# Kernel tuning notes

Hardware: AMD Instinct MI355X
Metric: run time of the kernel (lower is better)

## Reference

```python
import jax, jax.numpy as jnp
import numpy as np

NUM_HEADS = 32
HEAD_DIM = 128
ROPE_DIM = 64
HIDDEN = 4096
C_KV = 512
C_Q = 1536
CACHE_LEN = 4096
BATCH = 4


def _apply_rope(x, positions):
    # x: [B, S, H, R]; interleaved rotate-half RoPE at given absolute positions
    R = x.shape[-1]
    inv_freq = 1.0 / (10000.0 ** (jnp.arange(0, R, 2, dtype=jnp.float32) / R))
    ang = positions[:, None].astype(jnp.float32) * inv_freq[None, :]  # [S, R/2]
    cos = jnp.cos(ang)[None, :, None, :]
    sin = jnp.sin(ang)[None, :, None, :]
    x1, x2 = x[..., 0::2], x[..., 1::2]
    out = jnp.stack([x1 * cos - x2 * sin, x1 * sin + x2 * cos], axis=-1)
    return out.reshape(x.shape).astype(x.dtype)


def setup_inputs() -> dict:
    key = jax.random.key(0)
    ks = jax.random.split(key, 12)
    s = lambda fan: 1.0 / np.sqrt(fan)
    return {
        "hidden_states": jax.random.normal(ks[0], (BATCH, 1, HIDDEN), jnp.float32),
        "mask": jnp.zeros((BATCH, 1, 1, CACHE_LEN + 1), jnp.float32),
        "cached_c_KV": jax.random.normal(ks[1], (BATCH, CACHE_LEN, C_KV), jnp.float32),
        "cached_k_R": jax.random.normal(ks[2], (BATCH, CACHE_LEN, ROPE_DIM), jnp.float32),
        "W_DKV": jax.random.normal(ks[3], (HIDDEN, C_KV), jnp.float32) * s(HIDDEN),
        "W_UK": jax.random.normal(ks[4], (C_KV, NUM_HEADS * HEAD_DIM), jnp.float32) * s(C_KV),
        "W_UV": jax.random.normal(ks[5], (C_KV, NUM_HEADS * HEAD_DIM), jnp.float32) * s(C_KV),
        "W_DQ": jax.random.normal(ks[6], (HIDDEN, C_Q), jnp.float32) * s(HIDDEN),
        "W_UQ": jax.random.normal(ks[7], (C_Q, NUM_HEADS * HEAD_DIM), jnp.float32) * s(C_Q),
        "W_QR": jax.random.normal(ks[8], (C_Q, NUM_HEADS * ROPE_DIM), jnp.float32) * s(C_Q),
        "W_KR": jax.random.normal(ks[9], (HIDDEN, ROPE_DIM), jnp.float32) * s(HIDDEN),
        "W_O": jax.random.normal(ks[10], (NUM_HEADS * HEAD_DIM, HIDDEN), jnp.float32) * s(NUM_HEADS * HEAD_DIM),
    }


def reference(hidden_states, mask, cached_c_KV, cached_k_R,
              W_DKV, W_UK, W_UV, W_DQ, W_UQ, W_QR, W_KR, W_O):
    B = hidden_states.shape[0]
    S_cache = cached_c_KV.shape[1]
    scale = 1.0 / np.sqrt(HEAD_DIM + ROPE_DIM)

    # latent projections for current token
    c_KV = hidden_states @ W_DKV                      # [B,1,C_KV]
    k_C = (c_KV @ W_UK).reshape(B, 1, NUM_HEADS, HEAD_DIM)
    v_C = (c_KV @ W_UV).reshape(B, 1, NUM_HEADS, HEAD_DIM)
    c_Q = hidden_states @ W_DQ                        # [B,1,C_Q]
    q_C = (c_Q @ W_UQ).reshape(B, 1, NUM_HEADS, HEAD_DIM)
    q_R = (c_Q @ W_QR).reshape(B, 1, NUM_HEADS, ROPE_DIM)
    k_R = (hidden_states @ W_KR).reshape(B, 1, 1, ROPE_DIM)

    # RoPE at the current decode position (= cache length)
    pos = jnp.array([S_cache], dtype=jnp.int32)
    q_R = _apply_rope(q_R, pos)
    k_R_cur = _apply_rope(k_R, pos)
    k_R_cur = jnp.broadcast_to(k_R_cur, (B, 1, NUM_HEADS, ROPE_DIM))

    q = jnp.concatenate([q_C, q_R], axis=-1)          # [B,1,H,D+R]
    k_cur = jnp.concatenate([k_C, k_R_cur], axis=-1)  # [B,1,H,D+R]

    # re-up-project cached latents (the expensive MLA decode step)
    cached_k_C = (cached_c_KV @ W_UK).reshape(B, S_cache, NUM_HEADS, HEAD_DIM)
    cached_v_C = (cached_c_KV @ W_UV).reshape(B, S_cache, NUM_HEADS, HEAD_DIM)
    cached_k_R_exp = jnp.broadcast_to(cached_k_R[:, :, None, :],
                                      (B, S_cache, NUM_HEADS, ROPE_DIM))
    cached_k = jnp.concatenate([cached_k_C, cached_k_R_exp], axis=-1)

    k = jnp.concatenate([cached_k, k_cur], axis=1)    # [B,S+1,H,D+R]
    v = jnp.concatenate([cached_v_C, v_C], axis=1)    # [B,S+1,H,D]

    # single-query attention: scores [B,H,1,S+1]
    scores = jnp.einsum('bqhd,bkhd->bhqk', q, k) * scale
    scores = scores + mask * -1e9
    probs = jax.nn.softmax(scores, axis=-1)
    attn = jnp.einsum('bhqk,bkhd->bqhd', probs, v).reshape(B, 1, NUM_HEADS * HEAD_DIM)

    out = attn @ W_O                                  # [B,1,HIDDEN]
    new_cached_c_KV = jnp.concatenate([cached_c_KV, c_KV], axis=1)
    new_cached_k_R = jnp.concatenate([cached_k_R, k_R_cur[:, :, 0, :]], axis=1)
    return out, new_cached_c_KV, new_cached_k_R
```

## Files before the change

### kernel.cpp

```cpp
#include <hip/hip_runtime.h>
#include <math.h>

#define NB 4
#define HID 4096
#define CKV 512
#define CQ 1536
#define NH 32
#define HD 128
#define RD 64
#define SS 4096
#define SK 4097
#define SKP 4100

#define SCALE_F 0.07216878364870322f

#define NP1 64
#define NP2 24
#define NPV 32
#define NUV 16
#define NWO 32

#define KD   576
#define QKB_STR 584

typedef __attribute__((ext_vector_type(8))) short short8v;
typedef __attribute__((ext_vector_type(4))) float f32x4;

enum : int {
  WS_QABS  = 0,
  WS_QROPE = WS_QABS + NB*NH*CKV,
  WS_KROPE = WS_QROPE + NB*NH*RD,
  WS_CKV   = WS_KROPE + NB*RD,
  WS_CQ    = WS_CKV + NB*CKV,
  WS_SCA   = WS_CQ + NB*CQ,
  WS_P1    = WS_SCA + NB*NH*SKP,
  WS_P2    = WS_P1 + NP1*NB*528*4,
  WS_OPART = WS_P2 + NP2*NB*6144,
  WS_UVPART= WS_OPART + NPV*NB*NH*CKV,
  WS_WOPART= WS_UVPART + NUV*NB*HID,
  WS_KVBF  = WS_WOPART + NWO*NB*HID,
  WS_QBF   = WS_KVBF + (NB*SK*KD)/2,
  WS_TOTAL = WS_QBF + (NB*NH*KD)/2
};

__device__ inline void fma4(float4& a, float s, const float4& v) {
  a.x += s*v.x; a.y += s*v.y; a.z += s*v.z; a.w += s*v.w;
}
__device__ inline float dot4(const float4& a, const float4& b) {
  return a.x*b.x + a.y*b.y + a.z*b.z + a.w*b.w;
}
__device__ inline unsigned short f2bf(float f) {
  union { float f; unsigned int u; } v; v.f = f;
  unsigned int r = v.u + 0x7FFFu + ((v.u >> 16) & 1u);
  return (unsigned short)(r >> 16);
}
__device__ inline ushort4 f2bf4(float4 v) {
  ushort4 r; r.x = f2bf(v.x); r.y = f2bf(v.y); r.z = f2bf(v.z); r.w = f2bf(v.w);
  return r;
}

__global__ __launch_bounds__(256)
void k_proj1copy(const float* __restrict__ hidden,
                 const float* __restrict__ Wdkv,
                 const float* __restrict__ Wdq,
                 const float* __restrict__ Wkr,
                 float* __restrict__ ws,
                 const float4* __restrict__ src_ckv,
                 const float4* __restrict__ src_kr,
                 float4* __restrict__ dst_ckv,
                 float4* __restrict__ dst_kr) {
  __shared__ float4 red_s[4][NB][64];
  unsigned short* kvbf = (unsigned short*)(ws + WS_KVBF);
  const int bx = blockIdx.x;
  if (bx < 576) {
    const int gx = bx % 9, gy = bx / 9;
    const int lane = threadIdx.x & 63, ksub = threadIdx.x >> 6;
    const int col4 = gx * 64 + lane;
    const int k0 = gy * 64 + ksub * 16;
    const bool valid = col4 < 528;
    float4 acc[NB] = {};
    if (valid) {
      const float* W; int C4, wcol4;
      if (col4 < 128)      { W = Wdkv; C4 = 128; wcol4 = col4; }
      else if (col4 < 512) { W = Wdq;  C4 = 384; wcol4 = col4 - 128; }
      else                 { W = Wkr;  C4 = 16;  wcol4 = col4 - 512; }
      const float4* wp = (const float4*)W + (size_t)k0 * C4 + wcol4;
      #pragma unroll
      for (int i = 0; i < 16; ++i) {
        float4 w4 = wp[(size_t)i * C4];
        #pragma unroll
        for (int b = 0; b < NB; ++b) fma4(acc[b], hidden[b*HID + k0 + i], w4);
      }
    }
    #pragma unroll
    for (int b = 0; b < NB; ++b) red_s[ksub][b][lane] = acc[b];
    __syncthreads();
    if (ksub == 0 && valid) {
      #pragma unroll
      for (int b = 0; b < NB; ++b) {
        float4 s = red_s[0][b][lane];
        #pragma unroll
        for (int j = 1; j < 4; ++j) {
          float4 v = red_s[j][b][lane];
          s.x += v.x; s.y += v.y; s.z += v.z; s.w += v.w;
        }
        *(float4*)(ws + WS_P1 + ((size_t)(gy*NB + b)*528 + col4)*4) = s;
      }
    }
  } else {
    const int bxc = bx - 576;
    if (bxc < 8192) {
      int b = bxc >> 11;
      int idx = (bxc & 2047) * 256 + threadIdx.x;
      float4 v = src_ckv[(size_t)b*(SS*CKV/4) + idx];
      dst_ckv[(size_t)b*(SK*CKV/4) + idx] = v;
      int off = idx * 4;
      int k = off >> 9, c = off & 511;
      *(ushort4*)(kvbf + ((size_t)b*SK + k)*KD + c) = f2bf4(v);
    } else {
      int bx2 = bxc - 8192;
      int b = bx2 >> 8;
      int idx = (bx2 & 255) * 256 + threadIdx.x;
      float4 v = src_kr[(size_t)b*(SS*RD/4) + idx];
      dst_kr[(size_t)b*(SK*RD/4) + idx] = v;
      int off = idx * 4;
      int k = off >> 6, rr = off & 63;
      *(ushort4*)(kvbf + ((size_t)b*SK + k)*KD + 512 + rr) = f2bf4(v);
    }
  }
}

__global__ __launch_bounds__(256)
void k_proj2r1(const float* __restrict__ Wuq,
               const float* __restrict__ Wqr,
               float* __restrict__ ws,
               float* __restrict__ out_ckv,
               float* __restrict__ out_kr) {
  __shared__ float4 red_s[4][NB][64];
  __shared__ float act_s[NB][64];
  unsigned short* kvbf = (unsigned short*)(ws + WS_KVBF);
  const int bx = blockIdx.x;
  const int tid = threadIdx.x;
  if (bx < 576) {
    const int gx = bx % 24, gy = bx / 24;
    {
      const int b = tid >> 6, i = tid & 63;
      const int k = gy * 64 + i;
      const float* base = ws + WS_P1 + (size_t)b*2112 + 512 + k;
      float s = 0.f;
      #pragma unroll 8
      for (int p = 0; p < NP1; ++p) s += base[(size_t)p*NB*2112];
      act_s[b][i] = s;
    }
    __syncthreads();
    const int lane = tid & 63, ksub = tid >> 6;
    const int col4 = gx * 64 + lane;
    const float* W; int C4, wcol4;
    if (col4 < 1024) { W = Wuq; C4 = 1024; wcol4 = col4; }
    else             { W = Wqr; C4 = 512;  wcol4 = col4 - 1024; }
    const float4* wp = (const float4*)W + (size_t)(gy*64 + ksub*16) * C4 + wcol4;
    float4 acc[NB] = {};
    #pragma unroll
    for (int i = 0; i < 16; ++i) {
      float4 w4 = wp[(size_t)i * C4];
      #pragma unroll
      for (int b = 0; b < NB; ++b) fma4(acc[b], act_s[b][ksub*16 + i], w4);
    }
    #pragma unroll
    for (int b = 0; b < NB; ++b) red_s[ksub][b][lane] = acc[b];
    __syncthreads();
    if (ksub == 0) {
      #pragma unroll
      for (int b = 0; b < NB; ++b) {
        float4 s = red_s[0][b][lane];
        #pragma unroll
        for (int j = 1; j < 4; ++j) {
          float4 v = red_s[j][b][lane];
          s.x += v.x; s.y += v.y; s.z += v.z; s.w += v.w;
        }
        *(float4*)(ws + WS_P2 + (size_t)(gy*NB + b)*6144 + col4*4) = s;
      }
    }
  } else {
    const int w = (bx - 576) * 256 + tid;
    if (w >= 528*NB) return;
    const int b = w / 528, col4 = w % 528;
    float4 s = {};
    #pragma unroll 8
    for (int p = 0; p < NP1; ++p) {
      float4 v = *(const float4*)(ws + WS_P1 + ((size_t)(p*NB + b)*528 + col4)*4);
      s.x += v.x; s.y += v.y; s.z += v.z; s.w += v.w;
    }
    if (col4 < 128) {
      *(float4*)(ws + WS_CKV + b*CKV + col4*4) = s;
      *(float4*)(out_ckv + (size_t)b*SK*CKV + (size_t)SS*CKV + col4*4) = s;
      *(ushort4*)(kvbf + ((size_t)b*SK + SS)*KD + col4*4) = f2bf4(s);
    } else if (col4 < 512) {
      *(float4*)(ws + WS_CQ + b*CQ + (col4 - 128)*4) = s;
    } else {
      const int c0 = (col4 - 512) * 4;
      const double LN1E4 = 9.210340371976184;
      int i0 = c0 >> 1;
      double a0 = 4096.0 * exp(-(double)i0 / 32.0 * LN1E4);
      double a1 = 4096.0 * exp(-(double)(i0 + 1) / 32.0 * LN1E4);
      float c0f = (float)cos(a0), s0f = (float)sin(a0);
      float c1f = (float)cos(a1), s1f = (float)sin(a1);
      float4 o;
      o.x = s.x*c0f - s.y*s0f;  o.y = s.x*s0f + s.y*c0f;
      o.z = s.z*c1f - s.w*s1f;  o.w = s.z*s1f + s.w*c1f;
      *(float4*)(ws + WS_KROPE + b*RD + c0) = o;
      *(float4*)(out_kr + (size_t)b*SK*RD + (size_t)SS*RD + c0) = o;
      *(ushort4*)(kvbf + ((size_t)b*SK + SS)*KD + 512 + c0) = f2bf4(o);
    }
  }
}

__global__ __launch_bounds__(256)
void k_absorb_rope(const float* __restrict__ Wuk,
                   float* __restrict__ ws) {
  unsigned short* qbf = (unsigned short*)(ws + WS_QBF);
  const int bid = blockIdx.x, tid = threadIdx.x;
  if (bid < 256) {
    const int h = bid >> 3, cq = bid & 7;
    __shared__ float qc_s[NB][HD];
    __shared__ float part_s[NB][256];
    for (int e = tid; e < NB*HD; e += 256) {
      int b = e >> 7, d = e & 127;
      float v = 0.f;
      #pragma unroll
      for (int p = 0; p < NP2; ++p)
        v += ws[WS_P2 + (size_t)(p*NB + b)*6144 + h*HD + d];
      qc_s[b][d] = v;
    }
    __syncthreads();
    const int c = cq*64 + (tid & 63);
    const int dg = tid >> 6;
    const float4* wrow = (const float4*)(Wuk + (size_t)c*(NH*HD) + h*HD + dg*32);
    float acc[NB] = {0,0,0,0};
    #pragma unroll
    for (int d4 = 0; d4 < 8; ++d4) {
      float4 w4 = wrow[d4];
      #pragma unroll
      for (int b = 0; b < NB; ++b)
        acc[b] += dot4(w4, *(const float4*)&qc_s[b][dg*32 + d4*4]);
    }
    #pragma unroll
    for (int b = 0; b < NB; ++b) part_s[b][tid] = acc[b];
    __syncthreads();
    if (tid < 64) {
      #pragma unroll
      for (int b = 0; b < NB; ++b) {
        float v = (part_s[b][tid] + part_s[b][tid+64] + part_s[b][tid+128] + part_s[b][tid+192]) * SCALE_F;
        ws[WS_QABS + (size_t)(b*NH + h)*CKV + cq*64 + tid] = v;
        qbf[(size_t)(b*NH + h)*KD + cq*64 + tid] = f2bf(v);
      }
    }
  } else {
    const int b = bid - 256;
    const double LN1E4 = 9.210340371976184;
    for (int pid = tid; pid < NH*32; pid += 256) {
      int h = pid >> 5, i = pid & 31;
      float x1 = 0.f, x2 = 0.f;
      #pragma unroll
      for (int p = 0; p < NP2; ++p) {
        const float* base = ws + WS_P2 + (size_t)(p*NB + b)*6144 + 4096 + h*RD + 2*i;
        x1 += base[0]; x2 += base[1];
      }
      double ang = 4096.0 * exp(-(double)i / 32.0 * LN1E4);
      float cs = (float)cos(ang), sn = (float)sin(ang);
      float o0 = (x1*cs - x2*sn) * SCALE_F;
      float o1 = (x1*sn + x2*cs) * SCALE_F;
      ws[WS_QROPE + (b*NH + h)*RD + 2*i]     = o0;
      ws[WS_QROPE + (b*NH + h)*RD + 2*i + 1] = o1;
      qbf[(size_t)(b*NH + h)*KD + 512 + 2*i]     = f2bf(o0);
      qbf[(size_t)(b*NH + h)*KD + 512 + 2*i + 1] = f2bf(o1);
    }
  }
}

__global__ __launch_bounds__(256)
void k_scores_mfma(float* __restrict__ ws) {
  __shared__ unsigned short q_s[32 * QKB_STR];
  __shared__ unsigned short kv_s[32 * QKB_STR];
  const unsigned short* kvbf = (const unsigned short*)(ws + WS_KVBF);
  const unsigned short* qbf  = (const unsigned short*)(ws + WS_QBF);
  const int tid = threadIdx.x;
  const int b  = blockIdx.y;
  const int k0 = blockIdx.x * 32;
  {
    const int r = tid >> 3, u0 = tid & 7;
    const unsigned short* qsrc = qbf + (size_t)(b*NH + r)*KD;
    const int k = k0 + r;
    const unsigned short* ksrc = (k <= SS) ? (kvbf + ((size_t)b*SK + k)*KD) : nullptr;
    #pragma unroll
    for (int j = 0; j < 9; ++j) {
      int u = (u0 + 8*j) * 8;
      *(uint4*)&q_s[r*QKB_STR + u] = *(const uint4*)(qsrc + u);
      uint4 kvv = {0u, 0u, 0u, 0u};
      if (ksrc) kvv = *(const uint4*)(ksrc + u);
      *(uint4*)&kv_s[r*QKB_STR + u] = kvv;
    }
  }
  __syncthreads();
  const int wid = tid >> 6, lane = tid & 63;
  const int m0 = (wid & 1) * 16;
  const int n0 = (wid >> 1) * 16;
  const int l15 = lane & 15, lq = lane >> 4;
  const unsigned short* arow = &q_s[(m0 + l15)*QKB_STR + lq*8];
  const unsigned short* brow = &kv_s[(n0 + l15)*QKB_STR + lq*8];
  f32x4 acc = {0.f, 0.f, 0.f, 0.f};
  #pragma unroll
  for (int ks = 0; ks < 18; ++ks) {
    short8v a = *(const short8v*)(arow + ks*32);
    short8v bb = *(const short8v*)(brow + ks*32);
    acc = __builtin_amdgcn_mfma_f32_16x16x32_bf16(a, bb, acc, 0, 0, 0);
  }
  const int key = k0 + n0 + l15;
  if (key <= SS) {
    #pragma unroll
    for (int r = 0; r < 4; ++r) {
      int h = m0 + lq*4 + r;
      ws[WS_SCA + (size_t)(b*NH + h)*SKP + key] = acc[r];
    }
  }
}

__global__ __launch_bounds__(256)
void k_softmax(const float* __restrict__ mask, float* __restrict__ ws) {
  __shared__ float red[256];
  const int tid = threadIdx.x;
  const int b = blockIdx.x >> 5;
  float* sa = ws + WS_SCA + (size_t)blockIdx.x * SKP;
  const float* mrow = mask + (size_t)b * SK;
  float v[17];
  float m = -INFINITY;
  #pragma unroll
  for (int r = 0; r < 17; ++r) {
    int k = tid + r*256;
    v[r] = (k < SK) ? (sa[k] + mrow[k] * (-1e9f)) : -INFINITY;
    m = fmaxf(m, v[r]);
  }
  red[tid] = m; __syncthreads();
  for (int st = 128; st > 0; st >>= 1) {
    if (tid < st) red[tid] = fmaxf(red[tid], red[tid+st]);
    __syncthreads();
  }
  m = red[0]; __syncthreads();
  float e[17];
  float l = 0.f;
  #pragma unroll
  for (int r = 0; r < 17; ++r) {
    int k = tid + r*256;
    e[r] = (k < SK) ? __expf(v[r] - m) : 0.f;
    l += e[r];
  }
  red[tid] = l; __syncthreads();
  for (int st = 128; st > 0; st >>= 1) {
    if (tid < st) red[tid] += red[tid+st];
    __syncthreads();
  }
  float inv = 1.f / red[0];
  #pragma unroll
  for (int r = 0; r < 17; ++r) {
    int k = tid + r*256;
    if (k < SK) sa[k] = e[r] * inv;
  }
}

__global__ __launch_bounds__(256)
void k_pv(const float* __restrict__ kv_cache, float* __restrict__ ws) {
  __shared__ float p_s[32][132];
  const int tid = threadIdx.x;
  const int c4 = tid & 15, hg = tid >> 4;
  const int b  = blockIdx.z;
  const int c  = blockIdx.y * 64 + c4 * 4;
  const int k0 = blockIdx.x * 128;
  #pragma unroll
  for (int j = 0; j < 4; ++j) {
    int e = tid + j*256;
    int h = e >> 5, k4 = e & 31;
    *(float4*)&p_s[h][k4*4] =
        *(const float4*)(ws + WS_SCA + (size_t)(b*NH + h)*SKP + k0 + k4*4);
  }
  __syncthreads();
  const float* kvp = kv_cache + ((size_t)b*SS + k0)*CKV + c;
  float4 acc0 = {}, acc1 = {};
  #pragma unroll 4
  for (int kk = 0; kk < 128; kk += 4) {
    float4 kv4[4];
    #pragma unroll
    for (int j = 0; j < 4; ++j)
      kv4[j] = *(const float4*)(kvp + (size_t)(kk + j)*CKV);
    float4 p4a = *(const float4*)&p_s[hg][kk];
    float4 p4b = *(const float4*)&p_s[hg + 16][kk];
    fma4(acc0, p4a.x, kv4[0]); fma4(acc1, p4b.x, kv4[0]);
    fma4(acc0, p4a.y, kv4[1]); fma4(acc1, p4b.y, kv4[1]);
    fma4(acc0, p4a.z, kv4[2]); fma4(acc1, p4b.z, kv4[2]);
    fma4(acc0, p4a.w, kv4[3]); fma4(acc1, p4b.w, kv4[3]);
  }
  if (blockIdx.x == NPV - 1) {
    float4 kv = *(const float4*)(ws + WS_CKV + b*CKV + c);
    float pa = ws[WS_SCA + (size_t)(b*NH + hg)*SKP + SS];
    float pb = ws[WS_SCA + (size_t)(b*NH + hg + 16)*SKP + SS];
    fma4(acc0, pa, kv);
    fma4(acc1, pb, kv);
  }
  *(float4*)(ws + WS_OPART + (((size_t)blockIdx.x*NB + b)*NH + hg)*CKV + c) = acc0;
  *(float4*)(ws + WS_OPART + (((size_t)blockIdx.x*NB + b)*NH + hg + 16)*CKV + c) = acc1;
}

__global__ __launch_bounds__(256)
void k_uv2(const float* __restrict__ Wuv, float* __restrict__ ws) {
  __shared__ float4 red_s[4][NB][64];
  __shared__ float ol_s[NB][2][32];
  const int tid = threadIdx.x;
  const int x = blockIdx.x & 15, y = blockIdx.x >> 4;
  {
    const int b = tid >> 6, hh = (tid >> 5) & 1, ci = tid & 31;
    const float* base = ws + WS_OPART + ((size_t)b*NH + (2*x + hh))*CKV + y*32 + ci;
    float s = 0.f;
    #pragma unroll 8
    for (int p = 0; p < NPV; ++p) s += base[(size_t)p*(NB*NH*CKV)];
    ol_s[b][hh][ci] = s;
  }
  __syncthreads();
  const int lane = tid & 63, csub = tid >> 6;
  const int col4 = x * 64 + lane;
  const int hh = (col4 >> 5) & 1;
  const float4* wp = (const float4*)Wuv + (size_t)(y*32 + csub*8) * 1024 + col4;
  float4 acc[NB] = {};
  #pragma unroll
  for (int i = 0; i < 8; ++i) {
    float4 w4 = wp[(size_t)i * 1024];
    #pragma unroll
    for (int b = 0; b < NB; ++b)
      fma4(acc[b], ol_s[b][hh][csub*8 + i], w4);
  }
  #pragma unroll
  for (int b = 0; b < NB; ++b) red_s[csub][b][lane] = acc[b];
  __syncthreads();
  if (csub == 0) {
    #pragma unroll
    for (int b = 0; b < NB; ++b) {
      float4 s = red_s[0][b][lane];
      #pragma unroll
      for (int j = 1; j < 4; ++j) {
        float4 v = red_s[j][b][lane];
        s.x += v.x; s.y += v.y; s.z += v.z; s.w += v.w;
      }
      *(float4*)(ws + WS_UVPART + (size_t)(y*NB + b)*HID + col4*4) = s;
    }
  }
}

__global__ __launch_bounds__(256)
void k_wo2(const float* __restrict__ Wo, float* __restrict__ ws) {
  __shared__ float4 red_s[4][NB][64];
  __shared__ float at_s[NB][128];
  const int tid = threadIdx.x;
  const int x = blockIdx.x & 15, y = blockIdx.x >> 4;
  {
    const int b = tid >> 6, q = tid & 63;
    #pragma unroll
    for (int e = 0; e < 2; ++e) {
      int idx = q*2 + e;
      const float* base = ws + WS_UVPART + (size_t)b*HID + y*128 + idx;
      float s = 0.f;
      #pragma unroll
      for (int p = 0; p < NUV; ++p) s += base[(size_t)p*(NB*HID)];
      at_s[b][idx] = s;
    }
  }
  __syncthreads();
  const int lane = tid & 63, ksub = tid >> 6;
  const int col4 = x * 64 + lane;
  const float4* wp = (const float4*)Wo + (size_t)(y*128 + ksub*32) * 1024 + col4;
  float4 acc[NB] = {};
  #pragma unroll 8
  for (int i = 0; i < 32; ++i) {
    float4 w4 = wp[(size_t)i * 1024];
    #pragma unroll
    for (int b = 0; b < NB; ++b)
      fma4(acc[b], at_s[b][ksub*32 + i], w4);
  }
  #pragma unroll
  for (int b = 0; b < NB; ++b) red_s[ksub][b][lane] = acc[b];
  __syncthreads();
  if (ksub == 0) {
    #pragma unroll
    for (int b = 0; b < NB; ++b) {
      float4 s = red_s[0][b][lane];
      #pragma unroll
      for (int j = 1; j < 4; ++j) {
        float4 v = red_s[j][b][lane];
        s.x += v.x; s.y += v.y; s.z += v.z; s.w += v.w;
      }
      *(float4*)(ws + WS_WOPART + (size_t)(y*NB + b)*HID + col4*4) = s;
    }
  }
}

__global__ __launch_bounds__(256)
void k_reduce5(const float* __restrict__ ws, float* __restrict__ out) {
  const int idx = blockIdx.x * 256 + threadIdx.x;
  float4 s = {};
  #pragma unroll 8
  for (int p = 0; p < NWO; ++p) {
    float4 v = *(const float4*)(ws + WS_WOPART + (size_t)p*(NB*HID) + (size_t)idx*4);
    s.x += v.x; s.y += v.y; s.z += v.z; s.w += v.w;
  }
  *(float4*)(out + (size_t)idx*4) = s;
}

extern "C" void kernel_launch(void* const* d_in, const int* in_sizes, int n_in,
                              void* d_out, int out_size, void* d_ws, size_t ws_size,
                              hipStream_t stream) {
  (void)in_sizes; (void)n_in; (void)out_size; (void)ws_size;
  const float* hidden = (const float*)d_in[0];
  const float* mask   = (const float*)d_in[1];
  const float* ckv_c  = (const float*)d_in[2];
  const float* kr_c   = (const float*)d_in[3];
  const float* Wdkv   = (const float*)d_in[4];
  const float* Wuk    = (const float*)d_in[5];
  const float* Wuv    = (const float*)d_in[6];
  const float* Wdq    = (const float*)d_in[7];
  const float* Wuq    = (const float*)d_in[8];
  const float* Wqr    = (const float*)d_in[9];
  const float* Wkr    = (const float*)d_in[10];
  const float* Wo     = (const float*)d_in[11];
  float* out = (float*)d_out;
  float* ws  = (float*)d_ws;
  float* out_ckv = out + NB*HID;
  float* out_kr  = out + NB*HID + (size_t)NB*SK*CKV;

  k_proj1copy<<<9792, 256, 0, stream>>>(hidden, Wdkv, Wdq, Wkr, ws,
                                        (const float4*)ckv_c, (const float4*)kr_c,
                                        (float4*)out_ckv, (float4*)out_kr);
  k_proj2r1<<<585, 256, 0, stream>>>(Wuq, Wqr, ws, out_ckv, out_kr);
  k_absorb_rope<<<260, 256, 0, stream>>>(Wuk, ws);
  k_scores_mfma<<<dim3(129, 4), 256, 0, stream>>>(ws);
  k_softmax<<<NB*NH, 256, 0, stream>>>(mask, ws);
  k_pv<<<dim3(NPV, 8, 4), 256, 0, stream>>>(ckv_c, ws);
  k_uv2<<<256, 256, 0, stream>>>(Wuv, ws);
  k_wo2<<<512, 256, 0, stream>>>(Wo, ws);
  k_reduce5<<<16, 256, 0, stream>>>(ws, out);
}
```

Measured before the change: 112.6 us.

## Fuse scores, softmax and PV into split-K flash-decoding attention kernel

Replaces the separate scores, softmax and fp32 PV kernels with one kernel. Each block computes QK scores for a 128-key chunk with bf16 MFMA, does a local softmax, and multiplies P by the bf16 latent cache with MFMA, storing per-chunk max and sum. The UV kernel then rescales and combines the partial outputs. This removes the global score round-trip, two launches and the fp32 cache read in PV. In exchange, scores are recomputed once per column block (4x), and the probabilities and cache values are rounded to bf16.

```diff
diff --git a/kernel.cpp b/kernel.cpp
--- a/kernel.cpp
+++ b/kernel.cpp
@@ -22,6 +22,10 @@
 
 #define KD   576
 #define QKB_STR 584
+#define PBF_STR 4104
+#define TV_STR 40
+#define SFS  168
+#define PSTR 168
 
 typedef __attribute__((ext_vector_type(8))) short short8v;
 typedef __attribute__((ext_vector_type(4))) float f32x4;
@@ -40,7 +44,8 @@
   WS_WOPART= WS_UVPART + NUV*NB*HID,
   WS_KVBF  = WS_WOPART + NWO*NB*HID,
   WS_QBF   = WS_KVBF + (NB*SK*KD)/2,
-  WS_TOTAL = WS_QBF + (NB*NH*KD)/2
+  WS_ML    = WS_QBF + (NB*NH*KD)/2,
+  WS_TOTAL = WS_ML + NB*NH*NPV*2
 };
 
 __device__ inline void fma4(float4& a, float s, const float4& v) {
@@ -57,6 +62,10 @@
 __device__ inline ushort4 f2bf4(float4 v) {
   ushort4 r; r.x = f2bf(v.x); r.y = f2bf(v.y); r.z = f2bf(v.z); r.w = f2bf(v.w);
   return r;
+}
+__device__ inline float bf2f(unsigned short u) {
+  union { unsigned int u; float f; } v; v.u = ((unsigned int)u) << 16;
+  return v.f;
 }
 
 __global__ __launch_bounds__(256)
@@ -279,134 +288,138 @@
 }
 
 __global__ __launch_bounds__(256)
-void k_scores_mfma(float* __restrict__ ws) {
-  __shared__ unsigned short q_s[32 * QKB_STR];
+void k_attn(const float* __restrict__ mask, float* __restrict__ ws) {
   __shared__ unsigned short kv_s[32 * QKB_STR];
+  __shared__ float S_s[32 * SFS];
+  unsigned short* P_s  = kv_s;
+  unsigned short* kvT_s = kv_s + 32*PSTR;
   const unsigned short* kvbf = (const unsigned short*)(ws + WS_KVBF);
   const unsigned short* qbf  = (const unsigned short*)(ws + WS_QBF);
   const int tid = threadIdx.x;
-  const int b  = blockIdx.y;
-  const int k0 = blockIdx.x * 32;
-  {
-    const int r = tid >> 3, u0 = tid & 7;
-    const unsigned short* qsrc = qbf + (size_t)(b*NH + r)*KD;
-    const int k = k0 + r;
-    const unsigned short* ksrc = (k <= SS) ? (kvbf + ((size_t)b*SK + k)*KD) : nullptr;
-    #pragma unroll
-    for (int j = 0; j < 9; ++j) {
-      int u = (u0 + 8*j) * 8;
-      *(uint4*)&q_s[r*QKB_STR + u] = *(const uint4*)(qsrc + u);
-      uint4 kvv = {0u, 0u, 0u, 0u};
-      if (ksrc) kvv = *(const uint4*)(ksrc + u);
-      *(uint4*)&kv_s[r*QKB_STR + u] = kvv;
-    }
-  }
-  __syncthreads();
+  const int j  = blockIdx.x;
+  const int qy = blockIdx.y;
+  const int b  = blockIdx.z;
+  const int k0 = j * 128;
+  const int NSUB = (j == NPV-1) ? 5 : 4;
   const int wid = tid >> 6, lane = tid & 63;
+  const int l15 = lane & 15, lq = lane >> 4;
+
   const int m0 = (wid & 1) * 16;
   const int n0 = (wid >> 1) * 16;
-  const int l15 = lane & 15, lq = lane >> 4;
-  const unsigned short* arow = &q_s[(m0 + l15)*QKB_STR + lq*8];
-  const unsigned short* brow = &kv_s[(n0 + l15)*QKB_STR + lq*8];
-  f32x4 acc = {0.f, 0.f, 0.f, 0.f};
+  const unsigned short* arow = qbf + (size_t)(b*NH + m0 + l15)*KD + lq*8;
+  for (int sc = 0; sc < NSUB; ++sc) {
+    {
+      const int r = tid >> 3, u0 = tid & 7;
+      const int k = k0 + sc*32 + r;
+      const unsigned short* ksrc = (k <= SS) ? (kvbf + ((size_t)b*SK + k)*KD) : nullptr;
+      #pragma unroll
+      for (int u8 = 0; u8 < 9; ++u8) {
+        int u = (u0 + 8*u8) * 8;
+        uint4 kvv = {0u, 0u, 0u, 0u};
+        if (ksrc) kvv = *(const uint4*)(ksrc + u);
+        *(uint4*)&kv_s[r*QKB_STR + u] = kvv;
+      }
+    }
+    __syncthreads();
+    const unsigned short* brow = &kv_s[(n0 + l15)*QKB_STR + lq*8];
+    f32x4 acc = {0.f, 0.f, 0.f, 0.f};
+    #pragma unroll
+    for (int ks = 0; ks < 18; ++ks) {
+      short8v a = *(const short8v*)(arow + ks*32);
+      short8v bb = *(const short8v*)(brow + ks*32);
+      acc = __builtin_amdgcn_mfma_f32_16x16x32_bf16(a, bb, acc, 0, 0, 0);
+    }
+    const int kk = sc*32 + n0 + l15;
+    const bool vkey = (k0 + kk) <= SS;
+    #pragma unroll
+    for (int r = 0; r < 4; ++r)
+      S_s[(m0 + lq*4 + r)*SFS + kk] = vkey ? acc[r] : -1e30f;
+    __syncthreads();
+  }
+
+  {
+    const int row = tid >> 3, i8 = tid & 7;
+    const int NK = NSUB * 32;
+    float m = -INFINITY;
+    for (int kk = i8; kk < NK; kk += 8) {
+      int kgl = k0 + kk;
+      float mv = (kgl < SK) ? mask[(size_t)b*SK + kgl] : 0.f;
+      float v = S_s[row*SFS + kk] + mv * (-1e9f);
+      S_s[row*SFS + kk] = v;
+      m = fmaxf(m, v);
+    }
+    m = fmaxf(m, __shfl_xor(m, 1));
+    m = fmaxf(m, __shfl_xor(m, 2));
+    m = fmaxf(m, __shfl_xor(m, 4));
+    float l = 0.f;
+    for (int kk = i8; kk < NK; kk += 8) {
+      float e = __expf(S_s[row*SFS + kk] - m);
+      l += e;
+      P_s[row*PSTR + kk] = f2bf(e);
+    }
+    l += __shfl_xor(l, 1);
+    l += __shfl_xor(l, 2);
+    l += __shfl_xor(l, 4);
+    if (i8 == 0 && qy == 0) {
+      float* ml = ws + WS_ML + ((size_t)(b*NH + row)*NPV + j)*2;
+      ml[0] = m; ml[1] = l;
+    }
+  }
+  __syncthreads();
+
+  const int c0 = qy * 128;
+  f32x4 acc4[4] = {{0,0,0,0},{0,0,0,0},{0,0,0,0},{0,0,0,0}};
+  const int kk_st = tid & 31, cgrp = tid >> 5;
+  for (int sc = 0; sc < NSUB; ++sc) {
+    {
+      const int k = k0 + sc*32 + kk_st;
+      ushort4 v0 = {0,0,0,0}, v1 = {0,0,0,0}, v2 = {0,0,0,0}, v3 = {0,0,0,0};
+      if (k <= SS) {
+        const unsigned short* src = kvbf + ((size_t)b*SK + k)*KD + c0 + cgrp*16;
+        v0 = *(const ushort4*)(src);
+        v1 = *(const ushort4*)(src + 4);
+        v2 = *(const ushort4*)(src + 8);
+        v3 = *(const ushort4*)(src + 12);
+      }
+      int cb = cgrp*16;
+      kvT_s[(cb+ 0)*TV_STR + kk_st] = v0.x;
+      kvT_s[(cb+ 1)*TV_STR + kk_st] = v0.y;
+      kvT_s[(cb+ 2)*TV_STR + kk_st] = v0.z;
+      kvT_s[(cb+ 3)*TV_STR + kk_st] = v0.w;
+      kvT_s[(cb+ 4)*TV_STR + kk_st] = v1.x;
+      kvT_s[(cb+ 5)*TV_STR + kk_st] = v1.y;
+      kvT_s[(cb+ 6)*TV_STR + kk_st] = v1.z;
+      kvT_s[(cb+ 7)*TV_STR + kk_st] = v1.w;
+      kvT_s[(cb+ 8)*TV_STR + kk_st] = v2.x;
+      kvT_s[(cb+ 9)*TV_STR + kk_st] = v2.y;
+      kvT_s[(cb+10)*TV_STR + kk_st] = v2.z;
+      kvT_s[(cb+11)*TV_STR + kk_st] = v2.w;
+      kvT_s[(cb+12)*TV_STR + kk_st] = v3.x;
+      kvT_s[(cb+13)*TV_STR + kk_st] = v3.y;
+      kvT_s[(cb+14)*TV_STR + kk_st] = v3.z;
+      kvT_s[(cb+15)*TV_STR + kk_st] = v3.w;
+    }
+    __syncthreads();
+    short8v a = *(const short8v*)(&P_s[(m0 + l15)*PSTR + sc*32 + lq*8]);
+    #pragma unroll
+    for (int t = 0; t < 4; ++t) {
+      const int nt = (wid >> 1) + 2*t;
+      const unsigned short* brow = &kvT_s[(nt*16 + l15)*TV_STR + lq*8];
+      short8v bb = *(const short8v*)(brow);
+      acc4[t] = __builtin_amdgcn_mfma_f32_16x16x32_bf16(a, bb, acc4[t], 0, 0, 0);
+    }
+    __syncthreads();
+  }
   #pragma unroll
-  for (int ks = 0; ks < 18; ++ks) {
-    short8v a = *(const short8v*)(arow + ks*32);
-    short8v bb = *(const short8v*)(brow + ks*32);
-    acc = __builtin_amdgcn_mfma_f32_16x16x32_bf16(a, bb, acc, 0, 0, 0);
-  }
-  const int key = k0 + n0 + l15;
-  if (key <= SS) {
+  for (int t = 0; t < 4; ++t) {
+    const int nt = (wid >> 1) + 2*t;
+    const int c = c0 + nt*16 + l15;
     #pragma unroll
     for (int r = 0; r < 4; ++r) {
       int h = m0 + lq*4 + r;
-      ws[WS_SCA + (size_t)(b*NH + h)*SKP + key] = acc[r];
-    }
-  }
-}
-
-__global__ __launch_bounds__(256)
-void k_softmax(const float* __restrict__ mask, float* __restrict__ ws) {
-  __shared__ float red[256];
-  const int tid = threadIdx.x;
-  const int b = blockIdx.x >> 5;
-  float* sa = ws + WS_SCA + (size_t)blockIdx.x * SKP;
-  const float* mrow = mask + (size_t)b * SK;
-  float v[17];
-  float m = -INFINITY;
-  #pragma unroll
-  for (int r = 0; r < 17; ++r) {
-    int k = tid + r*256;
-    v[r] = (k < SK) ? (sa[k] + mrow[k] * (-1e9f)) : -INFINITY;
-    m = fmaxf(m, v[r]);
-  }
-  red[tid] = m; __syncthreads();
-  for (int st = 128; st > 0; st >>= 1) {
-    if (tid < st) red[tid] = fmaxf(red[tid], red[tid+st]);
-    __syncthreads();
-  }
-  m = red[0]; __syncthreads();
-  float e[17];
-  float l = 0.f;
-  #pragma unroll
-  for (int r = 0; r < 17; ++r) {
-    int k = tid + r*256;
-    e[r] = (k < SK) ? __expf(v[r] - m) : 0.f;
-    l += e[r];
-  }
-  red[tid] = l; __syncthreads();
-  for (int st = 128; st > 0; st >>= 1) {
-    if (tid < st) red[tid] += red[tid+st];
-    __syncthreads();
-  }
-  float inv = 1.f / red[0];
-  #pragma unroll
-  for (int r = 0; r < 17; ++r) {
-    int k = tid + r*256;
-    if (k < SK) sa[k] = e[r] * inv;
-  }
-}
-
-__global__ __launch_bounds__(256)
-void k_pv(const float* __restrict__ kv_cache, float* __restrict__ ws) {
-  __shared__ float p_s[32][132];
-  const int tid = threadIdx.x;
-  const int c4 = tid & 15, hg = tid >> 4;
-  const int b  = blockIdx.z;
-  const int c  = blockIdx.y * 64 + c4 * 4;
-  const int k0 = blockIdx.x * 128;
-  #pragma unroll
-  for (int j = 0; j < 4; ++j) {
-    int e = tid + j*256;
-    int h = e >> 5, k4 = e & 31;
-    *(float4*)&p_s[h][k4*4] =
-        *(const float4*)(ws + WS_SCA + (size_t)(b*NH + h)*SKP + k0 + k4*4);
-  }
-  __syncthreads();
-  const float* kvp = kv_cache + ((size_t)b*SS + k0)*CKV + c;
-  float4 acc0 = {}, acc1 = {};
-  #pragma unroll 4
-  for (int kk = 0; kk < 128; kk += 4) {
-    float4 kv4[4];
-    #pragma unroll
-    for (int j = 0; j < 4; ++j)
-      kv4[j] = *(const float4*)(kvp + (size_t)(kk + j)*CKV);
-    float4 p4a = *(const float4*)&p_s[hg][kk];
-    float4 p4b = *(const float4*)&p_s[hg + 16][kk];
-    fma4(acc0, p4a.x, kv4[0]); fma4(acc1, p4b.x, kv4[0]);
-    fma4(acc0, p4a.y, kv4[1]); fma4(acc1, p4b.y, kv4[1]);
-    fma4(acc0, p4a.z, kv4[2]); fma4(acc1, p4b.z, kv4[2]);
-    fma4(acc0, p4a.w, kv4[3]); fma4(acc1, p4b.w, kv4[3]);
-  }
-  if (blockIdx.x == NPV - 1) {
-    float4 kv = *(const float4*)(ws + WS_CKV + b*CKV + c);
-    float pa = ws[WS_SCA + (size_t)(b*NH + hg)*SKP + SS];
-    float pb = ws[WS_SCA + (size_t)(b*NH + hg + 16)*SKP + SS];
-    fma4(acc0, pa, kv);
-    fma4(acc1, pb, kv);
-  }
-  *(float4*)(ws + WS_OPART + (((size_t)blockIdx.x*NB + b)*NH + hg)*CKV + c) = acc0;
-  *(float4*)(ws + WS_OPART + (((size_t)blockIdx.x*NB + b)*NH + hg + 16)*CKV + c) = acc1;
+      ws[WS_OPART + (((size_t)j*NB + b)*NH + h)*CKV + c] = acc4[t][r];
+    }
+  }
 }
 
 __global__ __launch_bounds__(256)
@@ -417,11 +430,20 @@
   const int x = blockIdx.x & 15, y = blockIdx.x >> 4;
   {
     const int b = tid >> 6, hh = (tid >> 5) & 1, ci = tid & 31;
-    const float* base = ws + WS_OPART + ((size_t)b*NH + (2*x + hh))*CKV + y*32 + ci;
-    float s = 0.f;
+    const int h = 2*x + hh, c = y*32 + ci;
+    const float* ml = ws + WS_ML + (size_t)(b*NH + h)*NPV*2;
+    float M = -INFINITY;
     #pragma unroll 8
-    for (int p = 0; p < NPV; ++p) s += base[(size_t)p*(NB*NH*CKV)];
-    ol_s[b][hh][ci] = s;
+    for (int p = 0; p < NPV; ++p) M = fmaxf(M, ml[p*2]);
+    const float* base = ws + WS_OPART + ((size_t)b*NH + h)*CKV + c;
+    float s = 0.f, L = 0.f;
+    #pragma unroll 4
+    for (int p = 0; p < NPV; ++p) {
+      float w = __expf(ml[p*2] - M);
+      L += w * ml[p*2 + 1];
+      s += w * base[(size_t)p*(NB*NH*CKV)];
+    }
+    ol_s[b][hh][ci] = s / L;
   }
   __syncthreads();
   const int lane = tid & 63, csub = tid >> 6;
@@ -538,9 +560,7 @@
                                         (float4*)out_ckv, (float4*)out_kr);
   k_proj2r1<<<585, 256, 0, stream>>>(Wuq, Wqr, ws, out_ckv, out_kr);
   k_absorb_rope<<<260, 256, 0, stream>>>(Wuk, ws);
-  k_scores_mfma<<<dim3(129, 4), 256, 0, stream>>>(ws);
-  k_softmax<<<NB*NH, 256, 0, stream>>>(mask, ws);
-  k_pv<<<dim3(NPV, 8, 4), 256, 0, stream>>>(ckv_c, ws);
+  k_attn<<<dim3(NPV, 4, 4), 256, 0, stream>>>(mask, ws);
   k_uv2<<<256, 256, 0, stream>>>(Wuv, ws);
   k_wo2<<<512, 256, 0, stream>>>(Wo, ws);
   k_reduce5<<<16, 256, 0, stream>>>(ws, out);
```

Result: slower. 120.5 us (+7.0%).
